# Performance work log

Hardware: AMD Instinct MI355X
Metric: run time of the kernel (lower is better)

Reference implementation:

```python
import jax, jax.numpy as jnp
import numpy as np

N_NODES = 200000
N_EDGES = 200000
N_GRAPHS = 128
IN_FEATS, HID_FEATS, OUT_FEATS = 256, 128, 128


def gcn_conv(x, W, b, src, dst, n_nodes):
    """PyG-style GCNConv: add self-loops, symmetric deg^-1/2 normalization."""
    h = x @ W  # [N, out]
    # degree with self-loops: deg[i] = 1 + (# edges with target i)
    deg = 1.0 + jax.ops.segment_sum(jnp.ones(src.shape[0], x.dtype), dst,
                                    num_segments=n_nodes)
    dinv = jax.lax.rsqrt(deg)
    norm = dinv[src] * dinv[dst]  # per-edge coeff
    agg = jax.ops.segment_sum(h[src] * norm[:, None], dst, num_segments=n_nodes)
    agg = agg + h * (1.0 / deg)[:, None]  # self-loop contribution
    return agg + b


def setup_inputs() -> dict:
    key = jax.random.key(0)
    k = jax.random.split(key, 8)
    x = jax.random.normal(k[0], (N_NODES, IN_FEATS), jnp.float32)
    edge_index = jax.random.randint(k[1], (2, N_EDGES), 0, N_NODES)
    batch = jnp.sort(jax.random.randint(k[2], (N_NODES,), 0, N_GRAPHS))
    root_index = jax.random.randint(k[3], (N_GRAPHS,), 0, N_NODES)
    # GCNConv params (xavier-ish scale)
    W1 = jax.random.normal(k[4], (IN_FEATS, HID_FEATS), jnp.float32) * (2.0 / (IN_FEATS + HID_FEATS)) ** 0.5
    b1 = jnp.zeros((HID_FEATS,), jnp.float32)
    W2 = jax.random.normal(k[5], (HID_FEATS + IN_FEATS, OUT_FEATS), jnp.float32) * (2.0 / (HID_FEATS + IN_FEATS + OUT_FEATS)) ** 0.5
    b2 = jnp.zeros((OUT_FEATS,), jnp.float32)
    return {"x": x, "edge_index": edge_index, "batch": batch,
            "root_index": root_index, "W1": W1, "b1": b1, "W2": W2, "b2": b2}


def reference(x, edge_index, batch, root_index, W1, b1, W2, b2):
    src, dst = edge_index[0], edge_index[1]
    x1 = x  # raw input features
    h = gcn_conv(x, W1, b1, src, dst, N_NODES)  # conv1 -> [N, hid]
    x2 = h
    # root broadcast: root_extend[i] = x1[root_index[batch[i]]]
    root_extend = x1[root_index[batch]]  # [N, in]
    h = jnp.concatenate([h, root_extend], axis=1)  # [N, hid+in]
    h = jax.nn.relu(h)
    # F.dropout(training=self.training): eval mode -> identity
    h = gcn_conv(h, W2, b2, src, dst, N_NODES)  # conv2 -> [N, out]
    h = jax.nn.relu(h)
    root_extend2 = x2[root_index[batch]]  # [N, hid]
    h = jnp.concatenate([h, root_extend2], axis=1)  # [N, out+hid]
    # scatter_mean over graphs
    sums = jax.ops.segment_sum(h, batch, num_segments=N_GRAPHS)
    counts = jax.ops.segment_sum(jnp.ones((N_NODES,), h.dtype), batch,
                                 num_segments=N_GRAPHS)
    return sums / jnp.maximum(counts, 1.0)[:, None]  # [B, out+hid]
```

## Files before the change

### kernel.cpp

```cpp
#include <hip/hip_runtime.h>
#include <stddef.h>

constexpr int N_NODES = 200000;
constexpr int N_EDGES = 200000;
constexpr int N_GRAPHS = 128;
constexpr int IN_F = 256;
constexpr int HID_F = 128;
constexpr int OUT_F = 128;
constexpr int OUT_W = OUT_F + HID_F;
constexpr int SCAN_NB = (N_NODES + 1023) / 1024;

typedef __attribute__((ext_vector_type(8))) short short8;
typedef __attribute__((ext_vector_type(4))) float float4v;

__device__ __forceinline__ short f2bf(float f) {
    union { float f; unsigned u; } v; v.f = f;
    unsigned r = v.u + 0x7fffu + ((v.u >> 16) & 1u);
    return (short)(r >> 16);
}


__global__ void edge_prep_kernel(const int* __restrict__ dst, int* __restrict__ cntin, int E) {
    int e = blockIdx.x * blockDim.x + threadIdx.x;
    if (e < E) atomicAdd(&cntin[dst[e]], 1);
}

__global__ void dinv_kernel(const int* __restrict__ cntin, float* __restrict__ dinv, int n) {
    int i = blockIdx.x * blockDim.x + threadIdx.x;
    if (i < n) dinv[i] = rsqrtf(1.0f + (float)cntin[i]);
}


__global__ __launch_bounds__(1024) void scan_reduce_kernel(const int* __restrict__ cnt,
                                                           int* __restrict__ partial, int n) {
    __shared__ int sm[1024];
    int t = threadIdx.x;
    int i = blockIdx.x * 1024 + t;
    sm[t] = (i < n) ? cnt[i] : 0;
    __syncthreads();
    for (int ofs = 512; ofs > 0; ofs >>= 1) {
        if (t < ofs) sm[t] += sm[t + ofs];
        __syncthreads();
    }
    if (t == 0) partial[blockIdx.x] = sm[0];
}

__global__ void scan_base_kernel(int* __restrict__ partial, int nb) {
    __shared__ int sm[256];
    int t = threadIdx.x;
    sm[t] = (t < nb) ? partial[t] : 0;
    __syncthreads();
    for (int ofs = 1; ofs < 256; ofs <<= 1) {
        int v = (t >= ofs) ? sm[t - ofs] : 0;
        __syncthreads();
        sm[t] += v;
        __syncthreads();
    }
    if (t < nb) partial[t] = (t == 0) ? 0 : sm[t - 1];
}

__global__ __launch_bounds__(1024) void scan_final_kernel(const int* __restrict__ cnt,
                                                          const int* __restrict__ partial,
                                                          int* __restrict__ rp,
                                                          int* __restrict__ cur, int n) {
    __shared__ int sm[1024];
    int t = threadIdx.x;
    int i = blockIdx.x * 1024 + t;
    int v = (i < n) ? cnt[i] : 0;
    sm[t] = v;
    __syncthreads();
    for (int ofs = 1; ofs < 1024; ofs <<= 1) {
        int u = (t >= ofs) ? sm[t - ofs] : 0;
        __syncthreads();
        sm[t] += u;
        __syncthreads();
    }
    int base = partial[blockIdx.x];
    if (i < n) {
        int ex = base + sm[t] - v;
        rp[i] = ex;
        cur[i] = ex;
        if (i == n - 1) rp[n] = ex + v;
    }
}

__global__ void bucket_kernel(const int* __restrict__ src, const int* __restrict__ dst,
                              int* __restrict__ cur, int* __restrict__ adj, int E) {
    int e = blockIdx.x * blockDim.x + threadIdx.x;
    if (e < E) {
        int pos = atomicAdd(&cur[dst[e]], 1);
        adj[pos] = src[e];
    }
}

__global__ void bounds_kernel(const int* __restrict__ batch, int* __restrict__ start,
                              int* __restrict__ cnt, int n, int G) {
    __shared__ int s_start[N_GRAPHS + 1];
    int g = threadIdx.x;
    if (g < G) {
        int lo = 0, hi = n;
        while (lo < hi) {
            int mid = (lo + hi) >> 1;
            if (batch[mid] < g) lo = mid + 1; else hi = mid;
        }
        s_start[g] = lo;
        if (g == 0) s_start[G] = n;
    }
    __syncthreads();
    if (g < G) {
        start[g] = s_start[g];
        cnt[g] = s_start[g + 1] - s_start[g];
    }
}

__global__ void transpose_w_kernel(const float* __restrict__ W, short* __restrict__ Bt, int K) {
    int k = blockIdx.x;
    int n = threadIdx.x;
    Bt[(size_t)n * K + k] = f2bf(W[(size_t)k * 128 + n]);
}

__global__ void rootlin_kernel(const float* __restrict__ x, const int* __restrict__ root_index,
                               const float* __restrict__ W2, float* __restrict__ rootlin)
{
    int g = blockIdx.x;
    int f = threadIdx.x;
    int r = root_index[g];
    const float* xr = x + (size_t)r * IN_F;
    float acc = 0.f;
    for (int k = 0; k < IN_F; ++k) {
        float xv = fmaxf(xr[k], 0.f);
        acc += xv * W2[(size_t)(HID_F + k) * OUT_F + f];
    }
    rootlin[(size_t)g * OUT_F + f] = acc;
}

template<int KTOT, bool GATHER, bool ADDROOT>
__global__ __launch_bounds__(256) void mfma_gemm_kernel(
    const float* __restrict__ A, const short* __restrict__ Bt,
    float* __restrict__ outp,
    const float* __restrict__ dinv, const float* __restrict__ bvec,
    const float* __restrict__ rootlin, const int* __restrict__ batch,
    const int* __restrict__ rp, const int* __restrict__ adj)
{
    __shared__ __align__(16) short As[64][136];
    __shared__ __align__(16) short Bs[128][136];

    const int tid = threadIdx.x;
    const int wave = tid >> 6;
    const int lane = tid & 63;
    const int quad = lane >> 4;
    const int l16  = lane & 15;
    const int row0 = blockIdx.x * 64;

    float4v acc[8];
    #pragma unroll
    for (int c = 0; c < 8; ++c) acc[c] = (float4v){0.f, 0.f, 0.f, 0.f};

    const int arow = tid >> 2;
    const int ac8 = (tid & 3) * 8;
    const int bn = tid >> 1;
    const int bk = (tid & 1) * 64;

    for (int kb = 0; kb < KTOT / 128; ++kb) {
        {
            const short* bp = Bt + (size_t)bn * KTOT + kb * 128 + bk;
            #pragma unroll
            for (int j = 0; j < 8; ++j)
                *(short8*)&Bs[bn][bk + 8 * j] = *(const short8*)(bp + 8 * j);
        }
        if (GATHER) {
            const int row = row0 + arow;
            float4 s0[4], s1[4];
            const float* hp = A + (size_t)row * 128 + ac8;
            #pragma unroll
            for (int jj = 0; jj < 4; ++jj) {
                s0[jj] = *(const float4*)(hp + 32 * jj);
                s1[jj] = *(const float4*)(hp + 32 * jj + 4);
            }
            int e0 = rp[row], e1 = rp[row + 1];
            for (int e = e0; e < e1; ++e) {
                const float* q = A + (size_t)adj[e] * 128 + ac8;
                #pragma unroll
                for (int jj = 0; jj < 4; ++jj) {
                    float4 a = *(const float4*)(q + 32 * jj);
                    float4 b = *(const float4*)(q + 32 * jj + 4);
                    s0[jj].x += a.x; s0[jj].y += a.y; s0[jj].z += a.z; s0[jj].w += a.w;
                    s1[jj].x += b.x; s1[jj].y += b.y; s1[jj].z += b.z; s1[jj].w += b.w;
                }
            }
            float asc = dinv[row];
            #pragma unroll
            for (int jj = 0; jj < 4; ++jj) {
                const float* bv = bvec + ac8 + 32 * jj;
                short8 s;
                s[0] = f2bf(fmaxf(asc * s0[jj].x + bv[0], 0.f));
                s[1] = f2bf(fmaxf(asc * s0[jj].y + bv[1], 0.f));
                s[2] = f2bf(fmaxf(asc * s0[jj].z + bv[2], 0.f));
                s[3] = f2bf(fmaxf(asc * s0[jj].w + bv[3], 0.f));
                s[4] = f2bf(fmaxf(asc * s1[jj].x + bv[4], 0.f));
                s[5] = f2bf(fmaxf(asc * s1[jj].y + bv[5], 0.f));
                s[6] = f2bf(fmaxf(asc * s1[jj].z + bv[6], 0.f));
                s[7] = f2bf(fmaxf(asc * s1[jj].w + bv[7], 0.f));
                *(short8*)&As[arow][ac8 + 32 * jj] = s;
            }
        } else {
            const float* ap = A + (size_t)(row0 + arow) * KTOT + kb * 128 + ac8;
            #pragma unroll
            for (int jj = 0; jj < 4; ++jj) {
                float4 f0 = *(const float4*)(ap + 32 * jj);
                float4 f1 = *(const float4*)(ap + 32 * jj + 4);
                short8 s;
                s[0] = f2bf(f0.x); s[1] = f2bf(f0.y); s[2] = f2bf(f0.z); s[3] = f2bf(f0.w);
                s[4] = f2bf(f1.x); s[5] = f2bf(f1.y); s[6] = f2bf(f1.z); s[7] = f2bf(f1.w);
                *(short8*)&As[arow][ac8 + 32 * jj] = s;
            }
        }
        __syncthreads();
        #pragma unroll
        for (int ks = 0; ks < 4; ++ks) {
            short8 af = *(const short8*)&As[wave * 16 + l16][ks * 32 + quad * 8];
            #pragma unroll
            for (int c = 0; c < 8; ++c) {
                short8 bf = *(const short8*)&Bs[c * 16 + l16][ks * 32 + quad * 8];
                acc[c] = __builtin_amdgcn_mfma_f32_16x16x32_bf16(af, bf, acc[c], 0, 0, 0);
            }
        }
        __syncthreads();
    }

    #pragma unroll
    for (int r = 0; r < 4; ++r) {
        int row = row0 + wave * 16 + quad * 4 + r;
        float di = dinv[row];
        const float* rl = nullptr;
        if (ADDROOT) rl = rootlin + (size_t)batch[row] * 128;
        #pragma unroll
        for (int c = 0; c < 8; ++c) {
            int col = c * 16 + l16;
            float v = acc[c][r];
            if (ADDROOT) v += rl[col];
            outp[(size_t)row * 128 + col] = v * di;
        }
    }
}

__global__ void mean_kernel(const float* __restrict__ hs2, const float* __restrict__ hs1,
                            const float* __restrict__ dinv, const float* __restrict__ b1v,
                            const float* __restrict__ b2v, const int* __restrict__ root_index,
                            const int* __restrict__ cnt, const int* __restrict__ start,
                            const int* __restrict__ rp, const int* __restrict__ adj,
                            float* __restrict__ out, int chunks)
{
    int g = blockIdx.x;
    int c = blockIdx.y;
    int f = threadIdx.x;
    int s = start[g], n = cnt[g];
    int per = (n + chunks - 1) / chunks;
    int lo = s + c * per;
    int hi = min(s + n, lo + per);
    float bb = b2v[f];
    float accv = 0.f;
    for (int i = lo; i < hi; ++i) {
        float v = hs2[(size_t)i * 128 + f];
        int e0 = rp[i], e1 = rp[i + 1];
        for (int e = e0; e < e1; ++e)
            v += hs2[(size_t)adj[e] * 128 + f];
        accv += fmaxf(dinv[i] * v + bb, 0.f);
    }
    if (hi > lo)
        atomicAdd(&out[(size_t)g * OUT_W + f], accv / (float)max(n, 1));
    if (c == 0) {
        int r = root_index[g];
        float v = 0.f;
        if (n > 0) {
            v = hs1[(size_t)r * 128 + f];
            int e0 = rp[r], e1 = rp[r + 1];
            for (int e = e0; e < e1; ++e)
                v += hs1[(size_t)adj[e] * 128 + f];
            v = dinv[r] * v + b1v[f];
        }
        out[(size_t)g * OUT_W + HID_F + f] = v;
    }
}


static inline size_t align_up(size_t x, size_t a) { return (x + a - 1) / a * a; }

extern "C" void kernel_launch(void* const* d_in, const int* in_sizes, int n_in,
                              void* d_out, int out_size, void* d_ws, size_t ws_size,
                              hipStream_t stream) {
    const float* x = (const float*)d_in[0];
    const int* ei = (const int*)d_in[1];
    const int* batch = (const int*)d_in[2];
    const int* root = (const int*)d_in[3];
    const float* W1 = (const float*)d_in[4];
    const float* b1 = (const float*)d_in[5];
    const float* W2 = (const float*)d_in[6];
    const float* b2 = (const float*)d_in[7];
    float* out = (float*)d_out;

    const int* src = ei;
    const int* dst = ei + N_EDGES;

    char* ws = (char*)d_ws;
    size_t off = 0;
    const size_t NB = (size_t)N_NODES * 128 * sizeof(float);

    float* dinv = (float*)(ws + off);    off = align_up(off + (size_t)N_NODES * sizeof(float), 256);
    int* cnt = (int*)(ws + off);         off = align_up(off + N_GRAPHS * sizeof(int), 256);
    int* startv = (int*)(ws + off);      off = align_up(off + N_GRAPHS * sizeof(int), 256);
    float* rootlin = (float*)(ws + off); off = align_up(off + (size_t)N_GRAPHS * OUT_F * sizeof(float), 256);
    short* Bt1 = (short*)(ws + off);     off = align_up(off + (size_t)128 * IN_F * sizeof(short), 256);
    short* Bt2 = (short*)(ws + off);     off = align_up(off + (size_t)128 * HID_F * sizeof(short), 256);
    int* rowptr = (int*)(ws + off);      off = align_up(off + (size_t)(N_NODES + 1) * sizeof(int), 256);
    int* cursor = (int*)(ws + off);      off = align_up(off + (size_t)N_NODES * sizeof(int), 256);
    int* partial = (int*)(ws + off);     off = align_up(off + (size_t)SCAN_NB * sizeof(int), 256);
    int* adj = (int*)(ws + off);         off = align_up(off + (size_t)N_EDGES * sizeof(int), 256);
    float* hs1 = (float*)(ws + off);     off = align_up(off + NB, 256);
    float* hs2 = (float*)(ws + off);     off = align_up(off + NB, 256);
    (void)ws_size; (void)n_in; (void)in_sizes; (void)out_size;

    hipMemsetAsync(cursor, 0, (size_t)N_NODES * sizeof(int), stream);
    edge_prep_kernel<<<(N_EDGES + 255) / 256, 256, 0, stream>>>(dst, cursor, N_EDGES);
    dinv_kernel<<<(N_NODES + 255) / 256, 256, 0, stream>>>(cursor, dinv, N_NODES);
    scan_reduce_kernel<<<SCAN_NB, 1024, 0, stream>>>(cursor, partial, N_NODES);
    scan_base_kernel<<<1, 256, 0, stream>>>(partial, SCAN_NB);
    scan_final_kernel<<<SCAN_NB, 1024, 0, stream>>>(cursor, partial, rowptr, cursor, N_NODES);
    bucket_kernel<<<(N_EDGES + 255) / 256, 256, 0, stream>>>(src, dst, cursor, adj, N_EDGES);
    bounds_kernel<<<1, N_GRAPHS, 0, stream>>>(batch, startv, cnt, N_NODES, N_GRAPHS);

    transpose_w_kernel<<<IN_F, 128, 0, stream>>>(W1, Bt1, IN_F);
    transpose_w_kernel<<<HID_F, 128, 0, stream>>>(W2, Bt2, HID_F);
    rootlin_kernel<<<N_GRAPHS, OUT_F, 0, stream>>>(x, root, W2, rootlin);

    mfma_gemm_kernel<IN_F, false, false><<<N_NODES / 64, 256, 0, stream>>>(
        x, Bt1, hs1, dinv, nullptr, nullptr, nullptr, nullptr, nullptr);

    mfma_gemm_kernel<HID_F, true, true><<<N_NODES / 64, 256, 0, stream>>>(
        hs1, Bt2, hs2, dinv, b1, rootlin, batch, rowptr, adj);

    hipMemsetAsync(out, 0, (size_t)N_GRAPHS * OUT_W * sizeof(float), stream);
    dim3 mg(N_GRAPHS, 32);
    mean_kernel<<<mg, 128, 0, stream>>>(hs2, hs1, dinv, b1, b2, root, cnt, startv,
                                        rowptr, adj, out, 32);
}
```

Before: 475.4 us.

## Store intermediate node features in bf16 and fuse small setup kernels

Intermediate feature buffers hs1 and hs2 are now written and read as bf16 instead of fp32, which halves the bytes moved by the neighbour gathers in the second GEMM and the mean kernel. The dinv computation is folded into the scan_final kernel, and the two weight-transpose launches are merged into one. This cuts memory traffic and launch overhead, but adds rounding error to the aggregated features.

```diff
diff --git a/kernel.cpp b/kernel.cpp
--- a/kernel.cpp
+++ b/kernel.cpp
@@ -18,16 +18,15 @@
     unsigned r = v.u + 0x7fffu + ((v.u >> 16) & 1u);
     return (short)(r >> 16);
 }
+__device__ __forceinline__ float bf2f(unsigned short s) {
+    union { unsigned u; float f; } v; v.u = ((unsigned)s) << 16;
+    return v.f;
+}
 
 
 __global__ void edge_prep_kernel(const int* __restrict__ dst, int* __restrict__ cntin, int E) {
     int e = blockIdx.x * blockDim.x + threadIdx.x;
     if (e < E) atomicAdd(&cntin[dst[e]], 1);
-}
-
-__global__ void dinv_kernel(const int* __restrict__ cntin, float* __restrict__ dinv, int n) {
-    int i = blockIdx.x * blockDim.x + threadIdx.x;
-    if (i < n) dinv[i] = rsqrtf(1.0f + (float)cntin[i]);
 }
 
 
@@ -62,7 +61,8 @@
 __global__ __launch_bounds__(1024) void scan_final_kernel(const int* __restrict__ cnt,
                                                           const int* __restrict__ partial,
                                                           int* __restrict__ rp,
-                                                          int* __restrict__ cur, int n) {
+                                                          int* __restrict__ cur,
+                                                          float* __restrict__ dinv, int n) {
     __shared__ int sm[1024];
     int t = threadIdx.x;
     int i = blockIdx.x * 1024 + t;
@@ -80,6 +80,7 @@
         int ex = base + sm[t] - v;
         rp[i] = ex;
         cur[i] = ex;
+        dinv[i] = rsqrtf(1.0f + (float)v);
         if (i == n - 1) rp[n] = ex + v;
     }
 }
@@ -113,10 +114,16 @@
     }
 }
 
-__global__ void transpose_w_kernel(const float* __restrict__ W, short* __restrict__ Bt, int K) {
+__global__ void transpose_w_kernel(const float* __restrict__ W1, const float* __restrict__ W2,
+                                   short* __restrict__ Bt1, short* __restrict__ Bt2) {
     int k = blockIdx.x;
     int n = threadIdx.x;
-    Bt[(size_t)n * K + k] = f2bf(W[(size_t)k * 128 + n]);
+    if (k < IN_F) {
+        Bt1[(size_t)n * IN_F + k] = f2bf(W1[(size_t)k * 128 + n]);
+    } else {
+        int kk = k - IN_F;
+        Bt2[(size_t)n * HID_F + kk] = f2bf(W2[(size_t)kk * 128 + n]);
+    }
 }
 
 __global__ void rootlin_kernel(const float* __restrict__ x, const int* __restrict__ root_index,
@@ -136,8 +143,8 @@
 
 template<int KTOT, bool GATHER, bool ADDROOT>
 __global__ __launch_bounds__(256) void mfma_gemm_kernel(
-    const float* __restrict__ A, const short* __restrict__ Bt,
-    float* __restrict__ outp,
+    const void* __restrict__ Ap, const short* __restrict__ Bt,
+    unsigned short* __restrict__ outp,
     const float* __restrict__ dinv, const float* __restrict__ bvec,
     const float* __restrict__ rootlin, const int* __restrict__ batch,
     const int* __restrict__ rp, const int* __restrict__ adj)
@@ -169,23 +176,24 @@
                 *(short8*)&Bs[bn][bk + 8 * j] = *(const short8*)(bp + 8 * j);
         }
         if (GATHER) {
+            const unsigned short* A = (const unsigned short*)Ap;
             const int row = row0 + arow;
-            float4 s0[4], s1[4];
-            const float* hp = A + (size_t)row * 128 + ac8;
+            float sum[4][8];
+            const unsigned short* hp = A + (size_t)row * 128 + ac8;
             #pragma unroll
             for (int jj = 0; jj < 4; ++jj) {
-                s0[jj] = *(const float4*)(hp + 32 * jj);
-                s1[jj] = *(const float4*)(hp + 32 * jj + 4);
+                short8 h = *(const short8*)(hp + 32 * jj);
+                #pragma unroll
+                for (int q = 0; q < 8; ++q) sum[jj][q] = bf2f((unsigned short)h[q]);
             }
             int e0 = rp[row], e1 = rp[row + 1];
             for (int e = e0; e < e1; ++e) {
-                const float* q = A + (size_t)adj[e] * 128 + ac8;
+                const unsigned short* qp = A + (size_t)adj[e] * 128 + ac8;
                 #pragma unroll
                 for (int jj = 0; jj < 4; ++jj) {
-                    float4 a = *(const float4*)(q + 32 * jj);
-                    float4 b = *(const float4*)(q + 32 * jj + 4);
-                    s0[jj].x += a.x; s0[jj].y += a.y; s0[jj].z += a.z; s0[jj].w += a.w;
-                    s1[jj].x += b.x; s1[jj].y += b.y; s1[jj].z += b.z; s1[jj].w += b.w;
+                    short8 h = *(const short8*)(qp + 32 * jj);
+                    #pragma unroll
+                    for (int q = 0; q < 8; ++q) sum[jj][q] += bf2f((unsigned short)h[q]);
                 }
             }
             float asc = dinv[row];
@@ -193,17 +201,13 @@
             for (int jj = 0; jj < 4; ++jj) {
                 const float* bv = bvec + ac8 + 32 * jj;
                 short8 s;
-                s[0] = f2bf(fmaxf(asc * s0[jj].x + bv[0], 0.f));
-                s[1] = f2bf(fmaxf(asc * s0[jj].y + bv[1], 0.f));
-                s[2] = f2bf(fmaxf(asc * s0[jj].z + bv[2], 0.f));
-                s[3] = f2bf(fmaxf(asc * s0[jj].w + bv[3], 0.f));
-                s[4] = f2bf(fmaxf(asc * s1[jj].x + bv[4], 0.f));
-                s[5] = f2bf(fmaxf(asc * s1[jj].y + bv[5], 0.f));
-                s[6] = f2bf(fmaxf(asc * s1[jj].z + bv[6], 0.f));
-                s[7] = f2bf(fmaxf(asc * s1[jj].w + bv[7], 0.f));
+                #pragma unroll
+                for (int q = 0; q < 8; ++q)
+                    s[q] = f2bf(fmaxf(asc * sum[jj][q] + bv[q], 0.f));
                 *(short8*)&As[arow][ac8 + 32 * jj] = s;
             }
         } else {
+            const float* A = (const float*)Ap;
             const float* ap = A + (size_t)(row0 + arow) * KTOT + kb * 128 + ac8;
             #pragma unroll
             for (int jj = 0; jj < 4; ++jj) {
@@ -239,12 +243,13 @@
             int col = c * 16 + l16;
             float v = acc[c][r];
             if (ADDROOT) v += rl[col];
-            outp[(size_t)row * 128 + col] = v * di;
-        }
-    }
-}
-
-__global__ void mean_kernel(const float* __restrict__ hs2, const float* __restrict__ hs1,
+            outp[(size_t)row * 128 + col] = (unsigned short)f2bf(v * di);
+        }
+    }
+}
+
+__global__ void mean_kernel(const unsigned short* __restrict__ hs2,
+                            const unsigned short* __restrict__ hs1,
                             const float* __restrict__ dinv, const float* __restrict__ b1v,
                             const float* __restrict__ b2v, const int* __restrict__ root_index,
                             const int* __restrict__ cnt, const int* __restrict__ start,
@@ -261,10 +266,10 @@
     float bb = b2v[f];
     float accv = 0.f;
     for (int i = lo; i < hi; ++i) {
-        float v = hs2[(size_t)i * 128 + f];
+        float v = bf2f(hs2[(size_t)i * 128 + f]);
         int e0 = rp[i], e1 = rp[i + 1];
         for (int e = e0; e < e1; ++e)
-            v += hs2[(size_t)adj[e] * 128 + f];
+            v += bf2f(hs2[(size_t)adj[e] * 128 + f]);
         accv += fmaxf(dinv[i] * v + bb, 0.f);
     }
     if (hi > lo)
@@ -273,10 +278,10 @@
         int r = root_index[g];
         float v = 0.f;
         if (n > 0) {
-            v = hs1[(size_t)r * 128 + f];
+            v = bf2f(hs1[(size_t)r * 128 + f]);
             int e0 = rp[r], e1 = rp[r + 1];
             for (int e = e0; e < e1; ++e)
-                v += hs1[(size_t)adj[e] * 128 + f];
+                v += bf2f(hs1[(size_t)adj[e] * 128 + f]);
             v = dinv[r] * v + b1v[f];
         }
         out[(size_t)g * OUT_W + HID_F + f] = v;
@@ -304,7 +309,7 @@
 
     char* ws = (char*)d_ws;
     size_t off = 0;
-    const size_t NB = (size_t)N_NODES * 128 * sizeof(float);
+    const size_t NB16 = (size_t)N_NODES * 128 * sizeof(unsigned short);
 
     float* dinv = (float*)(ws + off);    off = align_up(off + (size_t)N_NODES * sizeof(float), 256);
     int* cnt = (int*)(ws + off);         off = align_up(off + N_GRAPHS * sizeof(int), 256);
@@ -316,21 +321,19 @@
     int* cursor = (int*)(ws + off);      off = align_up(off + (size_t)N_NODES * sizeof(int), 256);
     int* partial = (int*)(ws + off);     off = align_up(off + (size_t)SCAN_NB * sizeof(int), 256);
     int* adj = (int*)(ws + off);         off = align_up(off + (size_t)N_EDGES * sizeof(int), 256);
-    float* hs1 = (float*)(ws + off);     off = align_up(off + NB, 256);
-    float* hs2 = (float*)(ws + off);     off = align_up(off + NB, 256);
+    unsigned short* hs1 = (unsigned short*)(ws + off); off = align_up(off + NB16, 256);
+    unsigned short* hs2 = (unsigned short*)(ws + off); off = align_up(off + NB16, 256);
     (void)ws_size; (void)n_in; (void)in_sizes; (void)out_size;
 
     hipMemsetAsync(cursor, 0, (size_t)N_NODES * sizeof(int), stream);
     edge_prep_kernel<<<(N_EDGES + 255) / 256, 256, 0, stream>>>(dst, cursor, N_EDGES);
-    dinv_kernel<<<(N_NODES + 255) / 256, 256, 0, stream>>>(cursor, dinv, N_NODES);
     scan_reduce_kernel<<<SCAN_NB, 1024, 0, stream>>>(cursor, partial, N_NODES);
     scan_base_kernel<<<1, 256, 0, stream>>>(partial, SCAN_NB);
-    scan_final_kernel<<<SCAN_NB, 1024, 0, stream>>>(cursor, partial, rowptr, cursor, N_NODES);
+    scan_final_kernel<<<SCAN_NB, 1024, 0, stream>>>(cursor, partial, rowptr, cursor, dinv, N_NODES);
     bucket_kernel<<<(N_EDGES + 255) / 256, 256, 0, stream>>>(src, dst, cursor, adj, N_EDGES);
     bounds_kernel<<<1, N_GRAPHS, 0, stream>>>(batch, startv, cnt, N_NODES, N_GRAPHS);
 
-    transpose_w_kernel<<<IN_F, 128, 0, stream>>>(W1, Bt1, IN_F);
-    transpose_w_kernel<<<HID_F, 128, 0, stream>>>(W2, Bt2, HID_F);
+    transpose_w_kernel<<<IN_F + HID_F, 128, 0, stream>>>(W1, W2, Bt1, Bt2);
     rootlin_kernel<<<N_GRAPHS, OUT_F, 0, stream>>>(x, root, W2, rootlin);
 
     mfma_gemm_kernel<IN_F, false, false><<<N_NODES / 64, 256, 0, stream>>>(
```

Result: faster. 456.1 us (-4.1%).
